# Performance work log

Hardware: AMD Instinct MI355X
Metric: run time of the kernel (lower is better)

The kernel has to match this reference:

```python
import jax, jax.numpy as jnp
import numpy as np

N = 50000
E = 800000
N_CT = 32
EMBED = 256
HIDDEN = 128
OUT = 512
NEG_SLOPE = 0.2


def setup_inputs() -> dict:
    key = jax.random.key(0)
    ks = jax.random.split(key, 12)
    ct_idx = jax.random.randint(ks[0], (N,), 0, N_CT)
    cell_type_onehot = jax.nn.one_hot(ct_idx, N_CT, dtype=jnp.float32)
    lipid_droplet_scalar = jax.random.normal(ks[1], (N,), dtype=jnp.float32)
    edge_index = jax.random.randint(ks[2], (2, E), 0, N, dtype=jnp.int32)
    s = 0.05
    return {
        "cell_type_onehot": cell_type_onehot,
        "lipid_droplet_scalar": lipid_droplet_scalar,
        "edge_index": edge_index,
        "W_embed": jax.random.normal(ks[3], (N_CT + 1, EMBED), dtype=jnp.float32) * s,
        "b_embed": jnp.zeros((EMBED,), dtype=jnp.float32),
        "W_l": jax.random.normal(ks[4], (EMBED, HIDDEN), dtype=jnp.float32) * s,
        "b_l": jnp.zeros((HIDDEN,), dtype=jnp.float32),
        "W_r": jax.random.normal(ks[5], (EMBED, HIDDEN), dtype=jnp.float32) * s,
        "b_r": jnp.zeros((HIDDEN,), dtype=jnp.float32),
        "att": jax.random.normal(ks[6], (HIDDEN,), dtype=jnp.float32) * s,
        "gat_bias": jnp.zeros((HIDDEN,), dtype=jnp.float32),
        "W_out": jax.random.normal(ks[7], (HIDDEN, OUT), dtype=jnp.float32) * s,
        "b_out": jnp.zeros((OUT,), dtype=jnp.float32),
        "dispersion": jax.random.normal(ks[8], (OUT, N_CT), dtype=jnp.float32) * s,
    }


def reference(cell_type_onehot, lipid_droplet_scalar, edge_index,
              W_embed, b_embed, W_l, b_l, W_r, b_r, att, gat_bias,
              W_out, b_out, dispersion):
    n = cell_type_onehot.shape[0]
    lds = lipid_droplet_scalar[:, None] if lipid_droplet_scalar.ndim == 1 else lipid_droplet_scalar
    combined = jnp.concatenate([cell_type_onehot, lds], axis=1)  # [N, n_ct+1]
    x = jax.nn.elu(combined @ W_embed + b_embed)  # [N, EMBED]

    # GATv2Conv, heads=1, concat=True (PyG semantics)
    x_l = x @ W_l + b_l  # source-side transform [N, H]
    x_r = x @ W_r + b_r  # target-side transform [N, H]
    src, dst = edge_index[0], edge_index[1]
    e = jax.nn.leaky_relu(x_l[src] + x_r[dst], negative_slope=NEG_SLOPE)  # [E, H]
    logit = e @ att  # [E]
    # scatter-softmax over incoming edges of each target node
    m = jax.ops.segment_max(logit, dst, num_segments=n)
    alpha = jnp.exp(logit - m[dst])
    denom = jax.ops.segment_sum(alpha, dst, num_segments=n)
    alpha = alpha / (denom[dst] + 1e-16)
    agg = jax.ops.segment_sum(alpha[:, None] * x_l[src], dst, num_segments=n)  # [N, H]
    h = jax.nn.elu(agg + gat_bias)

    logits = h @ W_out + b_out  # [N, OUT]
    ct_idx = jnp.argmax(cell_type_onehot, axis=1)  # [N]
    disp = jax.nn.softplus(dispersion[:, ct_idx]).T  # [N, OUT]
    return logits, disp
```

## Files before the change

### kernel.cpp

```cpp
#include <hip/hip_runtime.h>
#include <hip/hip_bf16.h>
#include <math.h>

#define N    50000
#define E    800000
#define NCT  32
#define EMB  256
#define HID  128
#define OUTD 512
#define NB_SCAN 49

__device__ __forceinline__ float4 fma4s(float a, float4 b, float4 c) {
    return make_float4(fmaf(a, b.x, c.x), fmaf(a, b.y, c.y),
                       fmaf(a, b.z, c.z), fmaf(a, b.w, c.w));
}
__device__ __forceinline__ float4 add4(float4 a, float4 b) {
    return make_float4(a.x + b.x, a.y + b.y, a.z + b.z, a.w + b.w);
}

__global__ void k_init(const float* __restrict__ onehot,
                       const float* __restrict__ dispersion,
                       int* __restrict__ ct, int* __restrict__ hist,
                       float* __restrict__ spt) {
    int i = blockIdx.x * 256 + threadIdx.x;
    if (i < N) {
        const float* row = onehot + (size_t)i * NCT;
        int c = 0;
        #pragma unroll
        for (int j = 0; j < NCT; j++)
            if (row[j] > 0.5f) c = j;
        ct[i] = c;
        hist[i] = 0;
    }
    if (i < OUTD * NCT) {
        float x = dispersion[i];
        float s = log1pf(expf(-fabsf(x))) + fmaxf(x, 0.f);
        int c = i >> 5, j = i & 31;
        spt[j * OUTD + c] = s;
    }
}

__global__ __launch_bounds__(256) void k_embed(
        const int* __restrict__ ct, const float* __restrict__ ldsc,
        const float* __restrict__ We, const float* __restrict__ be,
        float* __restrict__ x) {
    int gid = blockIdx.x * 256 + threadIdx.x;
    if (gid >= N * (EMB / 4)) return;
    int n  = gid >> 6;
    int d  = (gid & 63) * 4;
    int c  = ct[n];
    float l = ldsc[n];
    float4 wc  = *reinterpret_cast<const float4*>(We + (size_t)c * EMB + d);
    float4 w32 = *reinterpret_cast<const float4*>(We + (size_t)NCT * EMB + d);
    float4 bb  = *reinterpret_cast<const float4*>(be + d);
    float4 v;
    v.x = fmaf(l, w32.x, wc.x) + bb.x;
    v.y = fmaf(l, w32.y, wc.y) + bb.y;
    v.z = fmaf(l, w32.z, wc.z) + bb.z;
    v.w = fmaf(l, w32.w, wc.w) + bb.w;
    v.x = v.x > 0.f ? v.x : expm1f(v.x);
    v.y = v.y > 0.f ? v.y : expm1f(v.y);
    v.z = v.z > 0.f ? v.z : expm1f(v.z);
    v.w = v.w > 0.f ? v.w : expm1f(v.w);
    *reinterpret_cast<float4*>(x + (size_t)n * EMB + d) = v;
}

__global__ __launch_bounds__(256) void k_hist(const int* __restrict__ eidx,
                                              int* __restrict__ hist) {
    int i = blockIdx.x * 256 + threadIdx.x;
    if (i < E / 4) {
        int4 d = reinterpret_cast<const int4*>(eidx + E)[i];
        atomicAdd(&hist[d.x], 1);
        atomicAdd(&hist[d.y], 1);
        atomicAdd(&hist[d.z], 1);
        atomicAdd(&hist[d.w], 1);
    }
}

__global__ __launch_bounds__(256, 4) void k_xlr(
        const float* __restrict__ x,
        const float* __restrict__ pWl, const float* __restrict__ pbl,
        const float* __restrict__ pWr, const float* __restrict__ pbr,
        float* __restrict__ xl, float* __restrict__ xr) {
    __shared__ float Bs[2][32 * HID];
    const int t  = threadIdx.x;
    const int b  = blockIdx.x & 1;
    const int n0 = (blockIdx.x >> 1) * 64;
    const float* Wp = b ? pWr : pWl;

    const int rg = t >> 5;
    const int cg = t & 31;
    const int c  = cg * 4;
    const int row0 = n0 + rg * 8;
    const float* xrow[8];
    #pragma unroll
    for (int r = 0; r < 8; r++) {
        int n = row0 + r; if (n >= N) n = N - 1;
        xrow[r] = x + (size_t)n * EMB;
    }
    const int st_kk  = t >> 5;
    const int st_col = (t & 31) * 4;

    float4 acc[8];
    #pragma unroll
    for (int r = 0; r < 8; r++) acc[r] = make_float4(0.f, 0.f, 0.f, 0.f);

    #pragma unroll
    for (int j = 0; j < 4; j++) {
        int kk = st_kk + j * 8;
        *reinterpret_cast<float4*>(&Bs[0][kk * HID + st_col]) =
            *reinterpret_cast<const float4*>(Wp + (size_t)kk * HID + st_col);
    }
    __syncthreads();

    for (int kc = 0; kc < EMB; kc += 32) {
        const int cur = (kc >> 5) & 1;
        if (kc + 32 < EMB) {
            #pragma unroll
            for (int j = 0; j < 4; j++) {
                int kk = st_kk + j * 8;
                *reinterpret_cast<float4*>(&Bs[cur ^ 1][kk * HID + st_col]) =
                    *reinterpret_cast<const float4*>(Wp + (size_t)(kc + 32 + kk) * HID + st_col);
            }
        }
        #pragma unroll
        for (int kk = 0; kk < 32; kk += 4) {
            float4 bq[4];
            #pragma unroll
            for (int q = 0; q < 4; q++)
                bq[q] = *reinterpret_cast<const float4*>(&Bs[cur][(kk + q) * HID + c]);
            float4 a[8];
            #pragma unroll
            for (int r = 0; r < 8; r++)
                a[r] = *reinterpret_cast<const float4*>(xrow[r] + kc + kk);
            #pragma unroll
            for (int r = 0; r < 8; r++) {
                acc[r] = fma4s(a[r].x, bq[0], acc[r]);
                acc[r] = fma4s(a[r].y, bq[1], acc[r]);
                acc[r] = fma4s(a[r].z, bq[2], acc[r]);
                acc[r] = fma4s(a[r].w, bq[3], acc[r]);
            }
        }
        __syncthreads();
    }

    float* outP = b ? xr : xl;
    const float4 bias = *reinterpret_cast<const float4*>((b ? pbr : pbl) + c);
    #pragma unroll
    for (int r = 0; r < 8; r++) {
        int n = row0 + r;
        if (n < N)
            *reinterpret_cast<float4*>(outP + (size_t)n * HID + c) = add4(acc[r], bias);
    }
}

__global__ __launch_bounds__(1024) void k_scan1(const int* __restrict__ hist,
                                                int* __restrict__ offs,
                                                int* __restrict__ bsum) {
    __shared__ int sb[2][1024];
    const int t = threadIdx.x;
    const int i = blockIdx.x * 1024 + t;
    int v = (i < N) ? hist[i] : 0;
    sb[0][t] = v;
    __syncthreads();
    int pin = 0;
    for (int off = 1; off < 1024; off <<= 1) {
        int x = sb[pin][t];
        if (t >= off) x += sb[pin][t - off];
        sb[pin ^ 1][t] = x;
        pin ^= 1;
        __syncthreads();
    }
    int incl = sb[pin][t];
    if (i < N) offs[i] = incl - v;
    if (t == 1023) bsum[blockIdx.x] = incl;
}

__global__ void k_scan2(const int* __restrict__ bsum, int* __restrict__ bbase) {
    if (threadIdx.x == 0) {
        int run = 0;
        for (int j = 0; j < NB_SCAN; j++) { bbase[j] = run; run += bsum[j]; }
    }
}

__global__ __launch_bounds__(1024) void k_scan3(int* __restrict__ offs,
                                                int* __restrict__ cursor,
                                                const int* __restrict__ bbase) {
    const int t = threadIdx.x;
    const int i = blockIdx.x * 1024 + t;
    if (i < N) {
        int v = offs[i] + bbase[blockIdx.x];
        offs[i] = v;
        cursor[i] = v;
    }
    if (blockIdx.x == 0 && t == 0) offs[N] = E;
}

__global__ __launch_bounds__(256) void k_scatter(const int* __restrict__ eidx,
                                                 int* __restrict__ cursor,
                                                 int* __restrict__ sorted) {
    const int e = blockIdx.x * 256 + threadIdx.x;
    if (e < E) {
        int s = eidx[e];
        int d = eidx[E + e];
        int pos = atomicAdd(&cursor[d], 1);
        sorted[pos] = s;
    }
}

__global__ __launch_bounds__(256, 8) void k_agg(
        const int* __restrict__ offs, const int* __restrict__ srt,
        const float* __restrict__ xl, const float* __restrict__ attv,
        const float* __restrict__ gb, float* xrh) {
    const int t = threadIdx.x;
    const int n = blockIdx.x * 8 + (t >> 5);
    if (n >= N) return;
    const int lane = t & 31;
    const float4* xl4 = reinterpret_cast<const float4*>(xl);
    float4* xh4 = reinterpret_cast<float4*>(xrh);

    const float4 xr4 = xh4[(size_t)n * 32 + lane];
    const float4 at4 = reinterpret_cast<const float4*>(attv)[lane];
    const int i0  = offs[n];
    const int deg = offs[n + 1] - i0;

    float m = -3.0e38f, den = 0.f;
    float4 acc = make_float4(0.f, 0.f, 0.f, 0.f);

#define STEP(XC) {                                                          \
    float vx = XC.x + xr4.x, vy = XC.y + xr4.y,                             \
          vz = XC.z + xr4.z, vw = XC.w + xr4.w;                             \
    vx = fmaxf(vx, 0.f) + 0.2f * fminf(vx, 0.f);                            \
    vy = fmaxf(vy, 0.f) + 0.2f * fminf(vy, 0.f);                            \
    vz = fmaxf(vz, 0.f) + 0.2f * fminf(vz, 0.f);                            \
    vw = fmaxf(vw, 0.f) + 0.2f * fminf(vw, 0.f);                            \
    float p = fmaf(vx, at4.x, fmaf(vy, at4.y, fmaf(vz, at4.z, vw * at4.w)));\
    p += __shfl_xor(p, 16); p += __shfl_xor(p, 8);                          \
    p += __shfl_xor(p, 4);  p += __shfl_xor(p, 2); p += __shfl_xor(p, 1);   \
    float mn = fmaxf(m, p);                                                 \
    float sc = __expf(m - mn);                                              \
    float w  = __expf(p - mn);                                              \
    den   = fmaf(den, sc, w);                                               \
    acc.x = fmaf(acc.x, sc, w * XC.x);                                      \
    acc.y = fmaf(acc.y, sc, w * XC.y);                                      \
    acc.z = fmaf(acc.z, sc, w * XC.z);                                      \
    acc.w = fmaf(acc.w, sc, w * XC.w);                                      \
    m = mn; }

    if (deg > 0) {
        const int lastI = i0 + deg - 1;
        #define LDX(J) xl4[(size_t)srt[min(i0 + (J), lastI)] * 32 + lane]
        float4 x0 = LDX(0), x1 = LDX(1), x2 = LDX(2), x3 = LDX(3);
        int i = 0;
        for (; i + 4 <= deg; i += 4) {
            const int base = i0 + i + 4;
            float4 n0 = xl4[(size_t)srt[min(base + 0, lastI)] * 32 + lane];
            float4 n1 = xl4[(size_t)srt[min(base + 1, lastI)] * 32 + lane];
            float4 n2 = xl4[(size_t)srt[min(base + 2, lastI)] * 32 + lane];
            float4 n3 = xl4[(size_t)srt[min(base + 3, lastI)] * 32 + lane];
            STEP(x0); STEP(x1); STEP(x2); STEP(x3);
            x0 = n0; x1 = n1; x2 = n2; x3 = n3;
        }
        if (i     < deg) STEP(x0);
        if (i + 1 < deg) STEP(x1);
        if (i + 2 < deg) STEP(x2);
        #undef LDX
    }
#undef STEP

    float inv = 1.f / (den + 1e-16f);
    const float4 g4 = reinterpret_cast<const float4*>(gb)[lane];
    float hx = fmaf(acc.x, inv, g4.x);
    float hy = fmaf(acc.y, inv, g4.y);
    float hz = fmaf(acc.z, inv, g4.z);
    float hw = fmaf(acc.w, inv, g4.w);
    hx = hx > 0.f ? hx : expm1f(hx);
    hy = hy > 0.f ? hy : expm1f(hy);
    hz = hz > 0.f ? hz : expm1f(hz);
    hw = hw > 0.f ? hw : expm1f(hw);
    xh4[(size_t)n * 32 + lane] = make_float4(hx, hy, hz, hw);
}

__global__ __launch_bounds__(256, 3) void k_out(
        const float* __restrict__ h, const int* __restrict__ ct,
        const float* __restrict__ Wo, const float* __restrict__ bo,
        const float* __restrict__ spt, float* __restrict__ out) {
    __shared__ float hs[32 * HID];
    __shared__ float Bs[16 * OUTD];
    __shared__ int ctl[32];
    const int t  = threadIdx.x;
    const int n0 = blockIdx.x * 32;

    if (t < 32) { int n = n0 + t; ctl[t] = ct[n < N ? n : N - 1]; }
    {
        const float4* h4 = reinterpret_cast<const float4*>(h);
        #pragma unroll
        for (int j = 0; j < 4; j++) {
            int fi  = t + j * 256;
            int row = fi >> 5;
            int k4  = (fi & 31) * 4;
            int n = n0 + row;
            float4 v = (n < N) ? h4[(size_t)n * 32 + (fi & 31)]
                               : make_float4(0.f, 0.f, 0.f, 0.f);
            *reinterpret_cast<float4*>(&hs[row * HID + k4]) = v;
        }
    }

    const int rg = t >> 6;
    const int cg = t & 63;
    const int c0 = cg * 4;
    const int c1 = 256 + cg * 4;
    const float* hrow = hs + rg * 8 * HID;
    const int st_kk  = t >> 7;
    const int st_col = (t & 127) * 4;

    float4 acc0[8], acc1[8];
    #pragma unroll
    for (int r = 0; r < 8; r++) {
        acc0[r] = make_float4(0.f, 0.f, 0.f, 0.f);
        acc1[r] = make_float4(0.f, 0.f, 0.f, 0.f);
    }

    for (int kc = 0; kc < HID; kc += 16) {
        __syncthreads();
        #pragma unroll
        for (int j = 0; j < 8; j++) {
            int kk = st_kk + j * 2;
            *reinterpret_cast<float4*>(&Bs[kk * OUTD + st_col]) =
                *reinterpret_cast<const float4*>(Wo + (size_t)(kc + kk) * OUTD + st_col);
        }
        __syncthreads();

        #pragma unroll
        for (int kk = 0; kk < 16; kk += 4) {
            float4 a[8];
            #pragma unroll
            for (int r = 0; r < 8; r++)
                a[r] = *reinterpret_cast<const float4*>(hrow + r * HID + kc + kk);
            #pragma unroll
            for (int q = 0; q < 4; q++) {
                float4 b0 = *reinterpret_cast<const float4*>(&Bs[(kk + q) * OUTD + c0]);
                float4 b1 = *reinterpret_cast<const float4*>(&Bs[(kk + q) * OUTD + c1]);
                const float* aq = reinterpret_cast<const float*>(a);
                #pragma unroll
                for (int r = 0; r < 8; r++) {
                    float av = aq[r * 4 + q];
                    acc0[r] = fma4s(av, b0, acc0[r]);
                    acc1[r] = fma4s(av, b1, acc1[r]);
                }
            }
        }
    }

    float* outd = out + (size_t)N * OUTD;
    const float4 bias0 = *reinterpret_cast<const float4*>(bo + c0);
    const float4 bias1 = *reinterpret_cast<const float4*>(bo + c1);
    #pragma unroll
    for (int r = 0; r < 8; r++) {
        int row = rg * 8 + r;
        int n = n0 + row;
        if (n < N) {
            *reinterpret_cast<float4*>(out + (size_t)n * OUTD + c0) = add4(acc0[r], bias0);
            *reinterpret_cast<float4*>(out + (size_t)n * OUTD + c1) = add4(acc1[r], bias1);
            int cn = ctl[row];
            *reinterpret_cast<float4*>(outd + (size_t)n * OUTD + c0) =
                *reinterpret_cast<const float4*>(spt + cn * OUTD + c0);
            *reinterpret_cast<float4*>(outd + (size_t)n * OUTD + c1) =
                *reinterpret_cast<const float4*>(spt + cn * OUTD + c1);
        }
    }
}

extern "C" void kernel_launch(void* const* d_in, const int* in_sizes, int n_in,
                              void* d_out, int out_size, void* d_ws, size_t ws_size,
                              hipStream_t stream) {
    const float* onehot     = (const float*)d_in[0];
    const float* ldsc       = (const float*)d_in[1];
    const int*   eidx       = (const int*)  d_in[2];
    const float* We         = (const float*)d_in[3];
    const float* be         = (const float*)d_in[4];
    const float* Wl         = (const float*)d_in[5];
    const float* bl         = (const float*)d_in[6];
    const float* Wr         = (const float*)d_in[7];
    const float* br         = (const float*)d_in[8];
    const float* attv       = (const float*)d_in[9];
    const float* gb         = (const float*)d_in[10];
    const float* Wo         = (const float*)d_in[11];
    const float* bo         = (const float*)d_in[12];
    const float* dispersion = (const float*)d_in[13];

    float* ws     = (float*)d_ws;
    float* xl     = ws;
    float* xr     = xl + (size_t)N * HID;
    int*   sorted = (int*)(xr + (size_t)N * HID);
    int*   ct     = sorted + E;
    int*   offs   = ct + N;
    int*   cursor = offs + (N + 1);
    int*   hist   = cursor + (N + 1);
    float* spt    = (float*)(hist + N);
    int*   bsum   = (int*)(spt + NCT * OUTD);
    int*   bbase  = bsum + 64;
    float* x      = (float*)(bbase + 64);

    float* out = (float*)d_out;

    const int xlr_tiles = (N + 63) / 64;

    k_init   <<<(N + 255) / 256, 256, 0, stream>>>(onehot, dispersion, ct, hist, spt);
    k_embed  <<<(N * (EMB / 4) + 255) / 256, 256, 0, stream>>>(ct, ldsc, We, be, x);
    k_hist   <<<(E / 4 + 255) / 256, 256, 0, stream>>>(eidx, hist);
    k_xlr    <<<xlr_tiles * 2, 256, 0, stream>>>(x, Wl, bl, Wr, br, xl, xr);
    k_scan1  <<<NB_SCAN, 1024, 0, stream>>>(hist, offs, bsum);
    k_scan2  <<<1, 64, 0, stream>>>(bsum, bbase);
    k_scan3  <<<NB_SCAN, 1024, 0, stream>>>(offs, cursor, bbase);
    k_scatter<<<(E + 255) / 256, 256, 0, stream>>>(eidx, cursor, sorted);
    k_agg    <<<(N + 7) / 8, 256, 0, stream>>>(offs, sorted, xl, attv, gb, xr);
    k_out    <<<(N + 31) / 32, 256, 0, stream>>>(xr, ct, Wo, bo, spt, out);
}
```

Baseline: 660.3 us.

## Fuse embedding into xl/xr GEMM and compute both projections per block

Drops the separate embedding kernel and the 50000x256 intermediate buffer x; each GEMM block now computes its 32 embedding rows straight into shared memory. The block also computes W_l and W_r together (256 output columns), so the embedding is built once per row instead of being read by two blocks. Shared memory use grows (32 KB for x plus 32 KB for the double-buffered weight tile), which may lower occupancy, and the K step shrinks from 32 to 16, doubling the number of barriers.

```diff
diff --git a/kernel.cpp b/kernel.cpp
--- a/kernel.cpp
+++ b/kernel.cpp
@@ -40,31 +40,6 @@
     }
 }
 
-__global__ __launch_bounds__(256) void k_embed(
-        const int* __restrict__ ct, const float* __restrict__ ldsc,
-        const float* __restrict__ We, const float* __restrict__ be,
-        float* __restrict__ x) {
-    int gid = blockIdx.x * 256 + threadIdx.x;
-    if (gid >= N * (EMB / 4)) return;
-    int n  = gid >> 6;
-    int d  = (gid & 63) * 4;
-    int c  = ct[n];
-    float l = ldsc[n];
-    float4 wc  = *reinterpret_cast<const float4*>(We + (size_t)c * EMB + d);
-    float4 w32 = *reinterpret_cast<const float4*>(We + (size_t)NCT * EMB + d);
-    float4 bb  = *reinterpret_cast<const float4*>(be + d);
-    float4 v;
-    v.x = fmaf(l, w32.x, wc.x) + bb.x;
-    v.y = fmaf(l, w32.y, wc.y) + bb.y;
-    v.z = fmaf(l, w32.z, wc.z) + bb.z;
-    v.w = fmaf(l, w32.w, wc.w) + bb.w;
-    v.x = v.x > 0.f ? v.x : expm1f(v.x);
-    v.y = v.y > 0.f ? v.y : expm1f(v.y);
-    v.z = v.z > 0.f ? v.z : expm1f(v.z);
-    v.w = v.w > 0.f ? v.w : expm1f(v.w);
-    *reinterpret_cast<float4*>(x + (size_t)n * EMB + d) = v;
-}
-
 __global__ __launch_bounds__(256) void k_hist(const int* __restrict__ eidx,
                                               int* __restrict__ hist) {
     int i = blockIdx.x * 256 + threadIdx.x;
@@ -78,79 +53,113 @@
 }
 
 __global__ __launch_bounds__(256, 4) void k_xlr(
-        const float* __restrict__ x,
+        const int* __restrict__ ct, const float* __restrict__ ldsc,
+        const float* __restrict__ We, const float* __restrict__ be,
         const float* __restrict__ pWl, const float* __restrict__ pbl,
         const float* __restrict__ pWr, const float* __restrict__ pbr,
         float* __restrict__ xl, float* __restrict__ xr) {
-    __shared__ float Bs[2][32 * HID];
+    __shared__ float xs[32 * EMB];
+    __shared__ float Bs[2][16 * 256];
+    __shared__ int   ctl[32];
+    __shared__ float ldl[32];
     const int t  = threadIdx.x;
-    const int b  = blockIdx.x & 1;
-    const int n0 = (blockIdx.x >> 1) * 64;
-    const float* Wp = b ? pWr : pWl;
-
-    const int rg = t >> 5;
-    const int cg = t & 31;
-    const int c  = cg * 4;
-    const int row0 = n0 + rg * 8;
-    const float* xrow[8];
-    #pragma unroll
-    for (int r = 0; r < 8; r++) {
-        int n = row0 + r; if (n >= N) n = N - 1;
-        xrow[r] = x + (size_t)n * EMB;
-    }
-    const int st_kk  = t >> 5;
-    const int st_col = (t & 31) * 4;
+    const int n0 = blockIdx.x * 32;
+
+    if (t < 32) {
+        int n = n0 + t; if (n >= N) n = N - 1;
+        ctl[t] = ct[n];
+        ldl[t] = ldsc[n];
+    }
+    __syncthreads();
+
+    #pragma unroll
+    for (int j = 0; j < 4; j++) {
+        int fi  = t + j * 256;
+        int kk  = fi >> 6;
+        int col = (fi & 63) * 4;
+        const float* src = (col < HID) ? (pWl + (size_t)kk * HID + col)
+                                       : (pWr + (size_t)kk * HID + col - HID);
+        *reinterpret_cast<float4*>(&Bs[0][kk * 256 + col]) =
+            *reinterpret_cast<const float4*>(src);
+    }
+    #pragma unroll
+    for (int j = 0; j < 8; j++) {
+        int fi  = t + j * 256;
+        int row = fi >> 6;
+        int col = (fi & 63) * 4;
+        float l = ldl[row];
+        float4 wc  = *reinterpret_cast<const float4*>(We + (size_t)ctl[row] * EMB + col);
+        float4 w32 = *reinterpret_cast<const float4*>(We + (size_t)NCT * EMB + col);
+        float4 bb  = *reinterpret_cast<const float4*>(be + col);
+        float4 v;
+        v.x = fmaf(l, w32.x, wc.x) + bb.x;
+        v.y = fmaf(l, w32.y, wc.y) + bb.y;
+        v.z = fmaf(l, w32.z, wc.z) + bb.z;
+        v.w = fmaf(l, w32.w, wc.w) + bb.w;
+        v.x = v.x > 0.f ? v.x : expm1f(v.x);
+        v.y = v.y > 0.f ? v.y : expm1f(v.y);
+        v.z = v.z > 0.f ? v.z : expm1f(v.z);
+        v.w = v.w > 0.f ? v.w : expm1f(v.w);
+        *reinterpret_cast<float4*>(&xs[row * EMB + col]) = v;
+    }
+    __syncthreads();
+
+    const int rg = t >> 6;
+    const int c  = (t & 63) * 4;
+    const float* xrow = xs + rg * 8 * EMB;
 
     float4 acc[8];
     #pragma unroll
     for (int r = 0; r < 8; r++) acc[r] = make_float4(0.f, 0.f, 0.f, 0.f);
 
-    #pragma unroll
-    for (int j = 0; j < 4; j++) {
-        int kk = st_kk + j * 8;
-        *reinterpret_cast<float4*>(&Bs[0][kk * HID + st_col]) =
-            *reinterpret_cast<const float4*>(Wp + (size_t)kk * HID + st_col);
-    }
-    __syncthreads();
-
-    for (int kc = 0; kc < EMB; kc += 32) {
-        const int cur = (kc >> 5) & 1;
-        if (kc + 32 < EMB) {
+    int cur = 0;
+    for (int kc = 0; kc < EMB; kc += 16) {
+        if (kc + 16 < EMB) {
             #pragma unroll
             for (int j = 0; j < 4; j++) {
-                int kk = st_kk + j * 8;
-                *reinterpret_cast<float4*>(&Bs[cur ^ 1][kk * HID + st_col]) =
-                    *reinterpret_cast<const float4*>(Wp + (size_t)(kc + 32 + kk) * HID + st_col);
+                int fi  = t + j * 256;
+                int kk  = fi >> 6;
+                int col = (fi & 63) * 4;
+                const float* src = (col < HID)
+                    ? (pWl + (size_t)(kc + 16 + kk) * HID + col)
+                    : (pWr + (size_t)(kc + 16 + kk) * HID + col - HID);
+                *reinterpret_cast<float4*>(&Bs[cur ^ 1][kk * 256 + col]) =
+                    *reinterpret_cast<const float4*>(src);
             }
         }
         #pragma unroll
-        for (int kk = 0; kk < 32; kk += 4) {
-            float4 bq[4];
-            #pragma unroll
-            for (int q = 0; q < 4; q++)
-                bq[q] = *reinterpret_cast<const float4*>(&Bs[cur][(kk + q) * HID + c]);
+        for (int kk = 0; kk < 16; kk += 4) {
             float4 a[8];
             #pragma unroll
             for (int r = 0; r < 8; r++)
-                a[r] = *reinterpret_cast<const float4*>(xrow[r] + kc + kk);
+                a[r] = *reinterpret_cast<const float4*>(xrow + r * EMB + kc + kk);
             #pragma unroll
-            for (int r = 0; r < 8; r++) {
-                acc[r] = fma4s(a[r].x, bq[0], acc[r]);
-                acc[r] = fma4s(a[r].y, bq[1], acc[r]);
-                acc[r] = fma4s(a[r].z, bq[2], acc[r]);
-                acc[r] = fma4s(a[r].w, bq[3], acc[r]);
+            for (int q = 0; q < 4; q++) {
+                float4 bq = *reinterpret_cast<const float4*>(&Bs[cur][(kk + q) * 256 + c]);
+                #pragma unroll
+                for (int r = 0; r < 8; r++)
+                    acc[r] = fma4s((&a[r].x)[q], bq, acc[r]);
             }
         }
         __syncthreads();
-    }
-
-    float* outP = b ? xr : xl;
-    const float4 bias = *reinterpret_cast<const float4*>((b ? pbr : pbl) + c);
+        cur ^= 1;
+    }
+
+    float* outP;
+    float4 bias;
+    int cc;
+    if (c < HID) {
+        outP = xl; cc = c;
+        bias = *reinterpret_cast<const float4*>(pbl + cc);
+    } else {
+        outP = xr; cc = c - HID;
+        bias = *reinterpret_cast<const float4*>(pbr + cc);
+    }
     #pragma unroll
     for (int r = 0; r < 8; r++) {
-        int n = row0 + r;
+        int n = n0 + rg * 8 + r;
         if (n < N)
-            *reinterpret_cast<float4*>(outP + (size_t)n * HID + c) = add4(acc[r], bias);
+            *reinterpret_cast<float4*>(outP + (size_t)n * HID + cc) = add4(acc[r], bias);
     }
 }
 
@@ -400,16 +409,12 @@
     float* spt    = (float*)(hist + N);
     int*   bsum   = (int*)(spt + NCT * OUTD);
     int*   bbase  = bsum + 64;
-    float* x      = (float*)(bbase + 64);
 
     float* out = (float*)d_out;
 
-    const int xlr_tiles = (N + 63) / 64;
-
     k_init   <<<(N + 255) / 256, 256, 0, stream>>>(onehot, dispersion, ct, hist, spt);
-    k_embed  <<<(N * (EMB / 4) + 255) / 256, 256, 0, stream>>>(ct, ldsc, We, be, x);
     k_hist   <<<(E / 4 + 255) / 256, 256, 0, stream>>>(eidx, hist);
-    k_xlr    <<<xlr_tiles * 2, 256, 0, stream>>>(x, Wl, bl, Wr, br, xl, xr);
+    k_xlr    <<<(N + 31) / 32, 256, 0, stream>>>(ct, ldsc, We, be, Wl, bl, Wr, br, xl, xr);
     k_scan1  <<<NB_SCAN, 1024, 0, stream>>>(hist, offs, bsum);
     k_scan2  <<<1, 64, 0, stream>>>(bsum, bbase);
     k_scan3  <<<NB_SCAN, 1024, 0, stream>>>(offs, cursor, bbase);
```

New measurement: 565.6 us. 14.3% less time.
